# Performance work log

Measured on AMD Instinct MI355X. Metric: run time of the kernel, lower is better.

Reference implementation:

```python
import jax, jax.numpy as jnp
import numpy as np

NUM_HEADS = 16
EMB_SIZE = 1024
HEAD_SIZE = 64


def setup_inputs() -> dict:
    key = jax.random.key(0)
    ks = jax.random.split(key, 9)
    H, E, D = NUM_HEADS, EMB_SIZE, HEAD_SIZE
    s = 1.0 / np.sqrt(E)
    X = jax.random.normal(ks[0], (4, 2048, E), dtype=jnp.float32)
    Wq = jax.random.uniform(ks[1], (H, E, D), jnp.float32, -s, s)
    Wk = jax.random.uniform(ks[2], (H, E, D), jnp.float32, -s, s)
    Wv = jax.random.uniform(ks[3], (H, E, D), jnp.float32, -s, s)
    bq = jax.random.uniform(ks[4], (H, D), jnp.float32, -s, s)
    bk = jax.random.uniform(ks[5], (H, D), jnp.float32, -s, s)
    bv = jax.random.uniform(ks[6], (H, D), jnp.float32, -s, s)
    so = 1.0 / np.sqrt(H * D)
    Wo = jax.random.uniform(ks[7], (H * D, E), jnp.float32, -so, so)
    bo = jax.random.uniform(ks[8], (E,), jnp.float32, -so, so)
    return {"X": X, "Wq": Wq, "Wk": Wk, "Wv": Wv, "bq": bq, "bk": bk, "bv": bv, "Wo": Wo, "bo": bo}


def reference(X, Wq, Wk, Wv, bq, bk, bv, Wo, bo):
    B, S, E = X.shape
    H, _, D = Wq.shape
    # per-head projections (batched over heads)
    q = jnp.einsum('bse,hed->bhsd', X, Wq) + bq[None, :, None, :]
    k = jnp.einsum('bse,hed->bhsd', X, Wk) + bk[None, :, None, :]
    v = jnp.einsum('bse,hed->bhsd', X, Wv) + bv[None, :, None, :]
    # causal scaled-dot-product attention
    scores = jnp.einsum('bhsd,bhtd->bhst', q, k) / jnp.sqrt(jnp.float32(D))
    causal = jnp.tril(jnp.ones((S, S), dtype=bool))
    scores = jnp.where(causal[None, None], scores, jnp.float32(-jnp.inf))
    probs = jax.nn.softmax(scores, axis=-1)
    out = jnp.einsum('bhst,bhtd->bhsd', probs, v)
    # concat heads (head h occupies slots [h*D:(h+1)*D]) then output proj
    concat = out.transpose(0, 2, 1, 3).reshape(B, S, H * D)
    # dropout is identity in eval mode
    return concat @ Wo + bo
```

## Files before the change

kernel.cpp:

```cpp
#include <hip/hip_runtime.h>
#include <stdint.h>


typedef float   f32x4  __attribute__((ext_vector_type(4)));
typedef __bf16  bf16x8 __attribute__((ext_vector_type(8)));
typedef short   short8 __attribute__((ext_vector_type(8)));
typedef unsigned short ushort4v __attribute__((ext_vector_type(4)));

typedef __attribute__((address_space(1))) void GV;
typedef __attribute__((address_space(3))) void LV;

#define DEVI static __device__ __forceinline__

DEVI unsigned short f2bf(float f){
  unsigned u = __float_as_uint(f);
  unsigned r = u + 0x7fffu + ((u>>16)&1u);
  return (unsigned short)(r>>16);
}

DEVI unsigned cvt_pk_bf16(float lo, float hi){
  unsigned r;
  asm("v_cvt_pk_bf16_f32 %0, %1, %2" : "=v"(r) : "v"(lo), "v"(hi));
  return r;
}

DEVI void permlane32_swap(unsigned &a, unsigned &b){
  asm volatile("v_permlane32_swap_b32 %0, %1" : "+v"(a), "+v"(b));
}
DEVI void permlane16_swap(unsigned &a, unsigned &b){
  asm volatile("v_permlane16_swap_b32 %0, %1" : "+v"(a), "+v"(b));
}

DEVI void gl_lds16(const void* g, void* l){
  __builtin_amdgcn_global_load_lds((GV*)g, (LV*)l, 16, 0, 0);
}

#define BAR() asm volatile("s_barrier" ::: "memory")

__global__ __launch_bounds__(256) void pack_x(const float* __restrict__ X,
                                              short* __restrict__ Xb){
  int i = blockIdx.x*256 + threadIdx.x;
  const float4* p = (const float4*)(X + (size_t)i*8);
  float4 a = p[0], b = p[1];
  short8 o;
  o[0]=(short)f2bf(a.x); o[1]=(short)f2bf(a.y); o[2]=(short)f2bf(a.z); o[3]=(short)f2bf(a.w);
  o[4]=(short)f2bf(b.x); o[5]=(short)f2bf(b.y); o[6]=(short)f2bf(b.z); o[7]=(short)f2bf(b.w);
  *(short8*)(Xb + (size_t)i*8) = o;
}

__global__ __launch_bounds__(256) void pack_wqkv(const float* __restrict__ Wq,
                                                 const float* __restrict__ Wk,
                                                 const float* __restrict__ Wv,
                                                 short* __restrict__ Wp){
  int t = blockIdx.x*256 + threadIdx.x;
  int n = t >> 7, kc = t & 127;
  int which = n >> 10, hd = n & 1023, h = hd >> 6, d = hd & 63;
  const float* W = which==0 ? Wq : (which==1 ? Wk : Wv);
  const float* src = W + ((size_t)h*1024 + kc*8)*64 + d;
  short8 o;
  #pragma unroll
  for (int j=0;j<8;++j) o[j] = (short)f2bf(src[(size_t)j*64]);
  *(short8*)(Wp + (size_t)n*1024 + kc*8) = o;
}

__global__ __launch_bounds__(256) void pack_wo(const float* __restrict__ Wo,
                                               short* __restrict__ WoT){
  int t = blockIdx.x*256 + threadIdx.x;
  int n = t >> 7, kc = t & 127;
  const float* src = Wo + (size_t)(kc*8)*1024 + n;
  short8 o;
  #pragma unroll
  for (int j=0;j<8;++j) o[j] = (short)f2bf(src[(size_t)j*1024]);
  *(short8*)(WoT + (size_t)n*1024 + kc*8) = o;
}

__global__ __launch_bounds__(512)
void gemm_qkv(const short* __restrict__ A, const short* __restrict__ Bt,
              const float* __restrict__ b0, const float* __restrict__ b1,
              const float* __restrict__ b2,
              short* __restrict__ Qb, short* __restrict__ Kb, short* __restrict__ Vtb)
{
  __shared__ __align__(16) char sm[2][65536];
  const int K2 = 2048;
  int t = threadIdx.x, lane = t & 63, wid = t >> 6;
  int wr = wid >> 2, wc = wid & 3;
  int l15 = lane & 15, l4 = lane >> 4;
  int swz = (blockIdx.x & 7) * 48 + (blockIdx.x >> 3);
  int bm = swz & 31, bn = swz >> 5;
  size_t abase = (size_t)bm * 256 * K2;
  size_t bbase = (size_t)bn * 256 * K2;

  f32x4 acc[8][4] = {};
  bf16x8 af[2][2];
  bf16x8 bfr[2][4];
  const char* sA; const char* sB;

  int srow8 = t >> 3;
  int szs0  = (t & 7) * 16;
  auto stA = [&](int kt, int ca, char* buf){
    int r = ca*64 + srow8;
    int zs = szs0 ^ ((r & 7) << 4);
    gl_lds16((const char*)A + abase + (size_t)r*K2 + kt*128 + zs,
             buf + ca*8192 + wid*1024);
  };
  auto stB = [&](int kt, int cb, char* buf){
    int r = cb*64 + srow8;
    int zs = szs0 ^ ((r & 7) << 4);
    gl_lds16((const char*)Bt + bbase + (size_t)r*K2 + kt*128 + zs,
             buf + 32768 + cb*8192 + wid*1024);
  };
  auto rdA = [&](int p){
    #pragma unroll
    for (int kk = 0; kk < 2; ++kk){
      int cb = kk*64 + l4*16;
      #pragma unroll
      for (int u = 0; u < 2; ++u){
        int ra = wr*128 + (2*p + u)*16 + l15;
        af[kk][u] = *(const bf16x8*)(sA + ra*128 + (cb ^ ((ra&7)<<4)));
      }
    }
  };
  auto rdB = [&](){
    #pragma unroll
    for (int kk = 0; kk < 2; ++kk){
      int cb = kk*64 + l4*16;
      #pragma unroll
      for (int j = 0; j < 4; ++j){
        int rb = wc*64 + j*16 + l15;
        bfr[kk][j] = *(const bf16x8*)(sB + rb*128 + (cb ^ ((rb&7)<<4)));
      }
    }
  };
  auto mmp = [&](int p){
    __builtin_amdgcn_s_setprio(1);
    #pragma unroll
    for (int kk = 0; kk < 2; ++kk)
      #pragma unroll
      for (int u = 0; u < 2; ++u)
        #pragma unroll
        for (int j = 0; j < 4; ++j)
          acc[2*p+u][j] = __builtin_amdgcn_mfma_f32_16x16x32_bf16(af[kk][u], bfr[kk][j],
                                                                  acc[2*p+u][j], 0, 0, 0);
    __builtin_amdgcn_s_setprio(0);
  };

  stB(0,0,sm[0]); stB(0,1,sm[0]); stB(0,2,sm[0]); stB(0,3,sm[0]);
  stA(0,0,sm[0]); stA(0,2,sm[0]); stA(0,1,sm[0]); stA(0,3,sm[0]);
  asm volatile("s_waitcnt vmcnt(2)" ::: "memory");
  BAR();

  for (int kt = 0; kt < 16; ++kt){
    sA = sm[kt & 1]; sB = sA + 32768;
    char* nb = sm[(kt + 1) & 1];
    bool st = kt < 15;
    rdB(); rdA(0);
    if (st){ stB(kt+1, 0, nb); stB(kt+1, 1, nb); }
    BAR(); mmp(0); BAR();
    rdA(1);
    if (st){ stB(kt+1, 2, nb); stB(kt+1, 3, nb);
             asm volatile("s_waitcnt vmcnt(4)" ::: "memory"); }
    else   { asm volatile("s_waitcnt vmcnt(0)" ::: "memory"); }
    BAR(); mmp(1); BAR();
    rdA(2);
    if (st){ stA(kt+1, 0, nb); stA(kt+1, 2, nb); }
    BAR(); mmp(2); BAR();
    rdA(3);
    if (st){ stA(kt+1, 1, nb); stA(kt+1, 3, nb);
             asm volatile("s_waitcnt vmcnt(2)" ::: "memory"); }
    BAR(); mmp(3); BAR();
  }

  #pragma unroll
  for (int i = 0; i < 8; ++i){
    int mbase = bm*256 + wr*128 + i*16 + l4*4;
    #pragma unroll
    for (int j = 0; j < 4; ++j){
      int n = bn*256 + wc*64 + j*16 + l15;
      int which = n >> 10, hd = n & 1023, h = hd >> 6, d = hd & 63;
      const float* bp = which==0 ? b0 : (which==1 ? b1 : b2);
      float bias = bp[hd];
      int b = mbase >> 11, sbase = mbase & 2047;
      size_t bh = (size_t)(b*16 + h);
      if (which == 2){
        ushort4v pv;
        #pragma unroll
        for (int r = 0; r < 4; ++r) pv[r] = f2bf(acc[i][j][r] + bias);
        *(ushort4v*)(Vtb + (bh*64 + d)*2048 + sbase) = pv;
      } else {
        short* dst = (which==0 ? Qb : Kb) + bh*2048*64;
        float sc = which==0 ? 0.18033688f : 1.0f;
        #pragma unroll
        for (int r = 0; r < 4; ++r)
          dst[(size_t)(sbase + r)*64 + d] = (short)f2bf((acc[i][j][r] + bias) * sc);
      }
    }
  }
}

__global__ __launch_bounds__(512)
void gemm_out(const short* __restrict__ A, const short* __restrict__ Bt,
              const float* __restrict__ b0, float* __restrict__ Out)
{
  __shared__ __align__(16) char sm[3][49152];
  const int K2 = 2048;
  int t = threadIdx.x, lane = t & 63, wid = t >> 6;
  int wr = wid >> 2, wc = wid & 3;
  int l15 = lane & 15, l4 = lane >> 4;
  int swz = (blockIdx.x & 7) * 32 + (blockIdx.x >> 3);
  int bm = swz & 63, bn = swz >> 6;
  size_t abase = (size_t)bm * 128 * K2;
  size_t bbase = (size_t)bn * 256 * K2;

  f32x4 acc[4][4] = {};
  const char* sA; const char* sB;
  bf16x8 af[4], bfr[4];

  auto stageA = [&](int kt, char* buf){
    int kb = kt * 128;
    #pragma unroll
    for (int c = 0; c < 2; ++c){
      int x = c*8192 + t*16;
      int r = x >> 7, z = x & 127;
      int zs = z ^ ((r & 7) << 4);
      gl_lds16((const char*)A + abase + (size_t)r*K2 + kb + zs, buf + c*8192 + wid*1024);
    }
  };
  auto stageB = [&](int kt, char* buf, int c0){
    int kb = kt * 128;
    #pragma unroll
    for (int c = 0; c < 2; ++c){
      int cc = c0 + c;
      int x = cc*8192 + t*16;
      int r = x >> 7, z = x & 127;
      int zs = z ^ ((r & 7) << 4);
      gl_lds16((const char*)Bt + bbase + (size_t)r*K2 + kb + zs, buf + 16384 + cc*8192 + wid*1024);
    }
  };
  auto rd_af = [&](int kk){
    int cb = kk*64 + l4*16;
    #pragma unroll
    for (int i = 0; i < 4; ++i){
      int ra = wr*64 + i*16 + l15;
      af[i] = *(const bf16x8*)(sA + ra*128 + (cb ^ ((ra&7)<<4)));
    }
  };
  auto rd_bf = [&](int kk, int j0){
    int cb = kk*64 + l4*16;
    #pragma unroll
    for (int j = 0; j < 2; ++j){
      int rb = wc*64 + (j0 + j)*16 + l15;
      bfr[j0 + j] = *(const bf16x8*)(sB + rb*128 + (cb ^ ((rb&7)<<4)));
    }
  };
  auto mm = [&](int j0){
    __builtin_amdgcn_s_setprio(1);
    #pragma unroll
    for (int i = 0; i < 4; ++i)
      #pragma unroll
      for (int j = 0; j < 2; ++j)
        acc[i][j0+j] = __builtin_amdgcn_mfma_f32_16x16x32_bf16(af[i], bfr[j0+j], acc[i][j0+j], 0, 0, 0);
    __builtin_amdgcn_s_setprio(0);
  };

  stageA(0, sm[0]); stageB(0, sm[0], 0); stageB(0, sm[0], 2);
  stageA(1, sm[1]); stageB(1, sm[1], 0); stageB(1, sm[1], 2);

  for (int kt = 0; kt < 16; ++kt){
    if (kt == 15) asm volatile("s_waitcnt vmcnt(0)" ::: "memory");
    else          asm volatile("s_waitcnt vmcnt(6)" ::: "memory");
    BAR();
    sA = sm[kt % 3]; sB = sA + 16384;
    char* nb = sm[(kt + 2) % 3];
    bool st = kt < 14;
    rd_af(0); rd_bf(0, 0);
    if (st) stageA(kt + 2, nb);
    BAR(); mm(0); BAR();
    rd_bf(0, 2);
    if (st) stageB(kt + 2, nb, 0);
    BAR(); mm(2); BAR();
    rd_af(1); rd_bf(1, 0);
    if (st) stageB(kt + 2, nb, 2);
    BAR(); mm(0); BAR();
    rd_bf(1, 2);
    BAR(); mm(2);
  }

  #pragma unroll
  for (int i = 0; i < 4; ++i){
    int mbase = bm*128 + wr*64 + i*16 + l4*4;
    #pragma unroll
    for (int j = 0; j < 4; ++j){
      int n = bn*256 + wc*64 + j*16 + l15;
      float bias = b0[n];
      #pragma unroll
      for (int r = 0; r < 4; ++r)
        Out[(size_t)(mbase + r)*1024 + n] = acc[i][j][r] + bias;
    }
  }
}

__global__ __launch_bounds__(256, 5)
void attn(const short* __restrict__ Qb, const short* __restrict__ Kb,
          const short* __restrict__ Vtb, short* __restrict__ Ob)
{
  __shared__ __align__(16) char smK[2][8192];
  __shared__ __align__(16) char smV[2][8192];
  int t = threadIdx.x, lane = t & 63, wid = t >> 6;
  int l15 = lane & 15, hi = lane >> 4;
  int hi16 = hi*16, hi4 = hi*4;
  int bh = blockIdx.x & 63;
  int qb = 31 - (blockIdx.x >> 6);
  int b = bh >> 4, h = bh & 15;
  int wq0 = qb*64 + wid*16;
  const char* Qh = (const char*)(Qb + (size_t)bh*2048*64);
  const char* Kh = (const char*)(Kb + (size_t)bh*2048*64);
  const char* Vh = (const char*)(Vtb + (size_t)bh*64*2048);

  bf16x8 vones;
  #pragma unroll
  for (int z = 0; z < 8; ++z) vones[z] = (__bf16)1.0f;

  bf16x8 qf[2];
  #pragma unroll
  for (int kk = 0; kk < 2; ++kk)
    qf[kk] = *(const bf16x8*)(Qh + (size_t)(wq0 + l15)*128 + kk*64 + hi16);

  f32x4 oacc[4] = {};
  f32x4 lacc = {};

  int nkt = qb + 1;

  #pragma unroll
  for (int c = 0; c < 2; ++c){
    int x = c*4096 + t*16;
    int r = x >> 7, z = x & 127;
    int zs = z ^ ((r & 7) << 4);
    gl_lds16(Kh + (size_t)r*128 + zs, smK[0] + c*4096 + wid*1024);
    gl_lds16(Vh + (size_t)r*4096 + zs, smV[0] + c*4096 + wid*1024);
  }
  __syncthreads();

  for (int kt = 0; kt < nkt; ++kt){
    int cur = kt & 1;
    if (kt + 1 < nkt){
      int nxt = cur ^ 1;
      #pragma unroll
      for (int c = 0; c < 2; ++c){
        int x = c*4096 + t*16;
        int r = x >> 7, z = x & 127;
        int zs = z ^ ((r & 7) << 4);
        gl_lds16(Kh + (size_t)(kt+1)*8192 + (size_t)r*128 + zs, smK[nxt] + c*4096 + wid*1024);
        gl_lds16(Vh + (size_t)r*4096 + (size_t)(kt+1)*128 + zs, smV[nxt] + c*4096 + wid*1024);
      }
    }
    const char* Kc = smK[cur];
    const char* Vc = smV[cur];
    int kbase = kt * 64;

    f32x4 sa[4];
    __builtin_amdgcn_s_setprio(1);
    #pragma unroll
    for (int nt = 0; nt < 4; ++nt){
      f32x4 a = {};
      #pragma unroll
      for (int kk = 0; kk < 2; ++kk){
        int rk = nt*16 + l15;
        bf16x8 kf = *(const bf16x8*)(Kc + rk*128 + ((kk*64 + hi16) ^ ((rk&7)<<4)));
        a = __builtin_amdgcn_mfma_f32_16x16x32_bf16(kf, qf[kk], a, 0, 0, 0);
      }
      sa[nt] = a;
    }
    __builtin_amdgcn_s_setprio(0);

    if (kt == qb){
      int qrow = wq0 + l15;
      #pragma unroll
      for (int nt = 0; nt < 4; ++nt)
        #pragma unroll
        for (int r = 0; r < 4; ++r)
          if (kbase + nt*16 + hi4 + r > qrow) sa[nt][r] = -1e30f;
    }

    unsigned pw[8];
    #pragma unroll
    for (int nt = 0; nt < 4; ++nt){
      float p0 = exp2f(sa[nt][0]);
      float p1 = exp2f(sa[nt][1]);
      float p2 = exp2f(sa[nt][2]);
      float p3 = exp2f(sa[nt][3]);
      pw[nt*2]   = cvt_pk_bf16(p0, p1);
      pw[nt*2+1] = cvt_pk_bf16(p2, p3);
    }

    union U { unsigned u[4]; bf16x8 v; } f0, f1;
    {
      unsigned a0 = pw[0], b0v = pw[2];
      permlane32_swap(a0, b0v); permlane16_swap(a0, b0v);
      unsigned a1 = pw[1], b1v = pw[3];
      permlane32_swap(a1, b1v); permlane16_swap(a1, b1v);
      f0.u[0] = a0; f0.u[1] = a1; f0.u[2] = b0v; f0.u[3] = b1v;
      unsigned a2 = pw[4], b2v = pw[6];
      permlane32_swap(a2, b2v); permlane16_swap(a2, b2v);
      unsigned a3 = pw[5], b3v = pw[7];
      permlane32_swap(a3, b3v); permlane16_swap(a3, b3v);
      f1.u[0] = a2; f1.u[1] = a3; f1.u[2] = b2v; f1.u[3] = b3v;
    }

    __builtin_amdgcn_s_setprio(1);
    #pragma unroll
    for (int kk = 0; kk < 2; ++kk){
      bf16x8 pf = kk ? f1.v : f0.v;
      lacc = __builtin_amdgcn_mfma_f32_16x16x32_bf16(vones, pf, lacc, 0, 0, 0);
      #pragma unroll
      for (int dt = 0; dt < 4; ++dt){
        int rv = dt*16 + l15;
        bf16x8 vf = *(const bf16x8*)(Vc + rv*128 + ((kk*64 + hi16) ^ ((rv&7)<<4)));
        oacc[dt] = __builtin_amdgcn_mfma_f32_16x16x32_bf16(vf, pf, oacc[dt], 0, 0, 0);
      }
    }
    __builtin_amdgcn_s_setprio(0);

    __syncthreads();
  }

  float inv = 1.0f / lacc[0];
  int srow = wq0 + l15;
  size_t rb = ((size_t)(b*2048 + srow))*1024 + h*64 + hi4;
  #pragma unroll
  for (int dt = 0; dt < 4; ++dt){
    unsigned w0 = cvt_pk_bf16(oacc[dt][0]*inv, oacc[dt][1]*inv);
    unsigned w1 = cvt_pk_bf16(oacc[dt][2]*inv, oacc[dt][3]*inv);
    *(unsigned long long*)(Ob + rb + dt*16) =
        ((unsigned long long)w1 << 32) | (unsigned long long)w0;
  }
}

extern "C" void kernel_launch(void* const* d_in, const int* in_sizes, int n_in,
                              void* d_out, int out_size, void* d_ws, size_t ws_size,
                              hipStream_t stream)
{
  const float* X  = (const float*)d_in[0];
  const float* Wq = (const float*)d_in[1];
  const float* Wk = (const float*)d_in[2];
  const float* Wv = (const float*)d_in[3];
  const float* bq = (const float*)d_in[4];
  const float* bk = (const float*)d_in[5];
  const float* bv = (const float*)d_in[6];
  const float* Wo = (const float*)d_in[7];
  const float* bo = (const float*)d_in[8];
  float* Out = (float*)d_out;

  char* ws = (char*)d_ws;
  short* Xbf  = (short*)(ws);
  short* Wp   = (short*)(ws + 16777216);
  short* WoT  = (short*)(ws + 23068672);
  short* Qb   = (short*)(ws + 25165824);
  short* Kb   = (short*)(ws + 41943040);
  short* Vtb  = (short*)(ws + 58720256);
  short* Ob   = (short*)(ws + 75497472);

  pack_x   <<<4096, 256, 0, stream>>>(X, Xbf);
  pack_wqkv<<<1536, 256, 0, stream>>>(Wq, Wk, Wv, Wp);
  pack_wo  <<< 512, 256, 0, stream>>>(Wo, WoT);

  gemm_qkv<<<384, 512, 0, stream>>>(Xbf, Wp, bq, bk, bv, Qb, Kb, Vtb);
  attn    <<<2048, 256, 0, stream>>>(Qb, Kb, Vtb, Ob);
  gemm_out<<<256, 512, 0, stream>>>(Ob, WoT, bo, Out);
}
```

Before: 189.0 us.

## Prefetch B tiles two steps ahead in QKV GEMM and fuse pack kernels

Restructures the QKV GEMM pipeline so B tiles are loaded two k-steps ahead into the buffer whose B data has already been read into registers, while A tiles are loaded one step ahead. It uses 128-row halves in LDS with adjusted swizzled addressing. It also merges the three fp32-to-bf16 pack kernels into one launch to cut launch overhead. The deeper prefetch relies on register-held B fragments to avoid overwriting live LDS data, and adds the launch_bounds min-blocks hint.

Result: slower. 194.4 us (+2.8%).

```diff
diff --git a/kernel.cpp b/kernel.cpp
--- a/kernel.cpp
+++ b/kernel.cpp
@@ -37,44 +37,44 @@
 
 #define BAR() asm volatile("s_barrier" ::: "memory")
 
-__global__ __launch_bounds__(256) void pack_x(const float* __restrict__ X,
-                                              short* __restrict__ Xb){
-  int i = blockIdx.x*256 + threadIdx.x;
-  const float4* p = (const float4*)(X + (size_t)i*8);
-  float4 a = p[0], b = p[1];
-  short8 o;
-  o[0]=(short)f2bf(a.x); o[1]=(short)f2bf(a.y); o[2]=(short)f2bf(a.z); o[3]=(short)f2bf(a.w);
-  o[4]=(short)f2bf(b.x); o[5]=(short)f2bf(b.y); o[6]=(short)f2bf(b.z); o[7]=(short)f2bf(b.w);
-  *(short8*)(Xb + (size_t)i*8) = o;
-}
-
-__global__ __launch_bounds__(256) void pack_wqkv(const float* __restrict__ Wq,
-                                                 const float* __restrict__ Wk,
-                                                 const float* __restrict__ Wv,
-                                                 short* __restrict__ Wp){
-  int t = blockIdx.x*256 + threadIdx.x;
-  int n = t >> 7, kc = t & 127;
-  int which = n >> 10, hd = n & 1023, h = hd >> 6, d = hd & 63;
-  const float* W = which==0 ? Wq : (which==1 ? Wk : Wv);
-  const float* src = W + ((size_t)h*1024 + kc*8)*64 + d;
-  short8 o;
-  #pragma unroll
-  for (int j=0;j<8;++j) o[j] = (short)f2bf(src[(size_t)j*64]);
-  *(short8*)(Wp + (size_t)n*1024 + kc*8) = o;
-}
-
-__global__ __launch_bounds__(256) void pack_wo(const float* __restrict__ Wo,
-                                               short* __restrict__ WoT){
-  int t = blockIdx.x*256 + threadIdx.x;
-  int n = t >> 7, kc = t & 127;
-  const float* src = Wo + (size_t)(kc*8)*1024 + n;
-  short8 o;
-  #pragma unroll
-  for (int j=0;j<8;++j) o[j] = (short)f2bf(src[(size_t)j*1024]);
-  *(short8*)(WoT + (size_t)n*1024 + kc*8) = o;
-}
-
-__global__ __launch_bounds__(512)
+__global__ __launch_bounds__(256)
+void pack_all(const float* __restrict__ X,
+              const float* __restrict__ Wq, const float* __restrict__ Wk,
+              const float* __restrict__ Wv, const float* __restrict__ Wo,
+              short* __restrict__ Xb, short* __restrict__ Wp,
+              short* __restrict__ WoT)
+{
+  int bid = blockIdx.x;
+  if (bid < 4096){
+    int i = bid*256 + threadIdx.x;
+    const float4* p = (const float4*)(X + (size_t)i*8);
+    float4 a = p[0], b = p[1];
+    short8 o;
+    o[0]=(short)f2bf(a.x); o[1]=(short)f2bf(a.y); o[2]=(short)f2bf(a.z); o[3]=(short)f2bf(a.w);
+    o[4]=(short)f2bf(b.x); o[5]=(short)f2bf(b.y); o[6]=(short)f2bf(b.z); o[7]=(short)f2bf(b.w);
+    *(short8*)(Xb + (size_t)i*8) = o;
+  } else if (bid < 5632){
+    int t = (bid - 4096)*256 + threadIdx.x;
+    int n = t >> 7, kc = t & 127;
+    int which = n >> 10, hd = n & 1023, h = hd >> 6, d = hd & 63;
+    const float* W = which==0 ? Wq : (which==1 ? Wk : Wv);
+    const float* src = W + ((size_t)h*1024 + kc*8)*64 + d;
+    short8 o;
+    #pragma unroll
+    for (int j=0;j<8;++j) o[j] = (short)f2bf(src[(size_t)j*64]);
+    *(short8*)(Wp + (size_t)n*1024 + kc*8) = o;
+  } else {
+    int t = (bid - 5632)*256 + threadIdx.x;
+    int n = t >> 7, kc = t & 127;
+    const float* src = Wo + (size_t)(kc*8)*1024 + n;
+    short8 o;
+    #pragma unroll
+    for (int j=0;j<8;++j) o[j] = (short)f2bf(src[(size_t)j*1024]);
+    *(short8*)(WoT + (size_t)n*1024 + kc*8) = o;
+  }
+}
+
+__global__ __launch_bounds__(512, 2)
 void gemm_qkv(const short* __restrict__ A, const short* __restrict__ Bt,
               const float* __restrict__ b0, const float* __restrict__ b1,
               const float* __restrict__ b2,
@@ -91,47 +91,57 @@
   size_t bbase = (size_t)bn * 256 * K2;
 
   f32x4 acc[8][4] = {};
-  bf16x8 af[2][2];
+  bf16x8 af[4];
   bf16x8 bfr[2][4];
   const char* sA; const char* sB;
 
-  int srow8 = t >> 3;
-  int szs0  = (t & 7) * 16;
-  auto stA = [&](int kt, int ca, char* buf){
-    int r = ca*64 + srow8;
-    int zs = szs0 ^ ((r & 7) << 4);
-    gl_lds16((const char*)A + abase + (size_t)r*K2 + kt*128 + zs,
-             buf + ca*8192 + wid*1024);
-  };
-  auto stB = [&](int kt, int cb, char* buf){
-    int r = cb*64 + srow8;
-    int zs = szs0 ^ ((r & 7) << 4);
-    gl_lds16((const char*)Bt + bbase + (size_t)r*K2 + kt*128 + zs,
-             buf + 32768 + cb*8192 + wid*1024);
-  };
-  auto rdA = [&](int p){
+  auto uA = [&](int T, int h){
+    char* dst = sm[T & 1] + h*16384;
+    #pragma unroll
+    for (int c = 0; c < 2; ++c){
+      int x = c*8192 + t*16;
+      int r = x >> 7, z = x & 127;
+      int zs = z ^ ((r & 7) << 4);
+      gl_lds16((const char*)A + abase + (size_t)(h*128 + r)*K2 + T*128 + zs,
+               dst + c*8192 + wid*1024);
+    }
+  };
+  auto uB = [&](int T, int h){
+    char* dst = sm[T & 1] + 32768 + h*16384;
+    #pragma unroll
+    for (int c = 0; c < 2; ++c){
+      int x = c*8192 + t*16;
+      int r = x >> 7, z = x & 127;
+      int zs = z ^ ((r & 7) << 4);
+      gl_lds16((const char*)Bt + bbase + (size_t)(h*128 + r)*K2 + T*128 + zs,
+               dst + c*8192 + wid*1024);
+    }
+  };
+  auto rdB = [&](){
     #pragma unroll
     for (int kk = 0; kk < 2; ++kk){
       int cb = kk*64 + l4*16;
       #pragma unroll
+      for (int j = 0; j < 4; ++j){
+        int rb = wc*64 + j*16 + l15;
+        int hb = rb >> 7, lr = rb & 127;
+        bfr[kk][j] = *(const bf16x8*)(sB + hb*16384 + lr*128 + (cb ^ ((lr&7)<<4)));
+      }
+    }
+  };
+  auto rdA = [&](int p){
+    #pragma unroll
+    for (int kk = 0; kk < 2; ++kk){
+      int cb = kk*64 + l4*16;
+      #pragma unroll
       for (int u = 0; u < 2; ++u){
         int ra = wr*128 + (2*p + u)*16 + l15;
-        af[kk][u] = *(const bf16x8*)(sA + ra*128 + (cb ^ ((ra&7)<<4)));
-      }
-    }
-  };
-  auto rdB = [&](){
-    #pragma unroll
-    for (int kk = 0; kk < 2; ++kk){
-      int cb = kk*64 + l4*16;
-      #pragma unroll
-      for (int j = 0; j < 4; ++j){
-        int rb = wc*64 + j*16 + l15;
-        bfr[kk][j] = *(const bf16x8*)(sB + rb*128 + (cb ^ ((rb&7)<<4)));
-      }
-    }
-  };
-  auto mmp = [&](int p){
+        int ha = ra >> 7, lr = ra & 127;
+        af[kk*2 + u] = *(const bf16x8*)(sA + ha*16384 + lr*128 + (cb ^ ((lr&7)<<4)));
+      }
+    }
+  };
+  auto mmq = [&](int p){
     __builtin_amdgcn_s_setprio(1);
     #pragma unroll
     for (int kk = 0; kk < 2; ++kk)
@@ -139,35 +149,34 @@
       for (int u = 0; u < 2; ++u)
         #pragma unroll
         for (int j = 0; j < 4; ++j)
-          acc[2*p+u][j] = __builtin_amdgcn_mfma_f32_16x16x32_bf16(af[kk][u], bfr[kk][j],
+          acc[2*p+u][j] = __builtin_amdgcn_mfma_f32_16x16x32_bf16(af[kk*2+u], bfr[kk][j],
                                                                   acc[2*p+u][j], 0, 0, 0);
     __builtin_amdgcn_s_setprio(0);
   };
 
-  stB(0,0,sm[0]); stB(0,1,sm[0]); stB(0,2,sm[0]); stB(0,3,sm[0]);
-  stA(0,0,sm[0]); stA(0,2,sm[0]); stA(0,1,sm[0]); stA(0,3,sm[0]);
-  asm volatile("s_waitcnt vmcnt(2)" ::: "memory");
+  uB(0,0); uB(0,1); uA(0,0); uA(0,1); uB(1,0); uB(1,1);
+  asm volatile("s_waitcnt vmcnt(4)" ::: "memory");
   BAR();
 
-  for (int kt = 0; kt < 16; ++kt){
-    sA = sm[kt & 1]; sB = sA + 32768;
-    char* nb = sm[(kt + 1) & 1];
-    bool st = kt < 15;
+  for (int T = 0; T < 16; ++T){
+    sA = sm[T & 1]; sB = sA + 32768;
+    bool s1 = T < 15, s2 = T < 14;
     rdB(); rdA(0);
-    if (st){ stB(kt+1, 0, nb); stB(kt+1, 1, nb); }
-    BAR(); mmp(0); BAR();
+    if (s1) uA(T+1, 0);
+    BAR(); mmq(0); BAR();
     rdA(1);
-    if (st){ stB(kt+1, 2, nb); stB(kt+1, 3, nb);
-             asm volatile("s_waitcnt vmcnt(4)" ::: "memory"); }
-    else   { asm volatile("s_waitcnt vmcnt(0)" ::: "memory"); }
-    BAR(); mmp(1); BAR();
+    if (s1) uA(T+1, 1);
+    if (s2) uB(T+2, 0);
+    BAR(); mmq(1); BAR();
     rdA(2);
-    if (st){ stA(kt+1, 0, nb); stA(kt+1, 2, nb); }
-    BAR(); mmp(2); BAR();
+    if (s2) uB(T+2, 1);
+    BAR(); mmq(2); BAR();
     rdA(3);
-    if (st){ stA(kt+1, 1, nb); stA(kt+1, 3, nb);
-             asm volatile("s_waitcnt vmcnt(2)" ::: "memory"); }
-    BAR(); mmp(3); BAR();
+    if (s1){
+      if (T == 14) asm volatile("s_waitcnt vmcnt(0)" ::: "memory");
+      else         asm volatile("s_waitcnt vmcnt(4)" ::: "memory");
+    }
+    BAR(); mmq(3); BAR();
   }
 
   #pragma unroll
@@ -459,9 +468,7 @@
   short* Vtb  = (short*)(ws + 58720256);
   short* Ob   = (short*)(ws + 75497472);
 
-  pack_x   <<<4096, 256, 0, stream>>>(X, Xbf);
-  pack_wqkv<<<1536, 256, 0, stream>>>(Wq, Wk, Wv, Wp);
-  pack_wo  <<< 512, 256, 0, stream>>>(Wo, WoT);
+  pack_all<<<6144, 256, 0, stream>>>(X, Wq, Wk, Wv, Wo, Xbf, Wp, WoT);
 
   gemm_qkv<<<384, 512, 0, stream>>>(Xbf, Wp, bq, bk, bv, Qb, Kb, Vtb);
   attn    <<<2048, 256, 0, stream>>>(Qb, Kb, Vtb, Ob);
```
